# Kernel tuning notes

Measured on AMD Instinct MI355X. Metric: run time of the kernel, lower is better.

Reference implementation:

```python
import jax, jax.numpy as jnp
import numpy as np

B, T, D = 4, 2048, 2048
H = 16
HO = D // H  # head_out = 128


def setup_inputs() -> dict:
    key = jax.random.key(0)
    ks = jax.random.split(key, 6)
    x = jax.random.normal(ks[0], (B, T, D), dtype=jnp.float32)
    scale = 0.02
    Wq = jax.random.normal(ks[1], (D, D), dtype=jnp.float32) * scale
    Wk = jax.random.normal(ks[2], (D, D), dtype=jnp.float32) * scale
    Wv = jax.random.normal(ks[3], (D, D), dtype=jnp.float32) * scale
    Wp = jax.random.normal(ks[4], (D, D), dtype=jnp.float32) * scale
    bp = jnp.zeros((D,), dtype=jnp.float32)
    return {"x": x, "Wq": Wq, "Wk": Wk, "Wv": Wv, "Wp": Wp, "bp": bp}


def reference(x, Wq, Wk, Wv, Wp, bp):
    b, t, _ = x.shape
    # QKV projections (weights stored [d_in, d_out])
    q = x @ Wq
    k = x @ Wk
    v = x @ Wv
    split = lambda a: a.reshape(b, t, H, HO).transpose(0, 2, 1, 3)  # [b,H,T,ho]
    qh, kh, vh = split(q), split(k), split(v)
    # Feature attention: contract over tokens -> [b,H,ho,ho]
    scores = jnp.einsum('bhtf,bhtg->bhfg', qh, kh) / jnp.sqrt(jnp.float32(HO))
    weights = jax.nn.softmax(scores, axis=-1)  # dropout p=0.0 (identity)
    # feature_alibi: [1/T, 1/(T-1), ..., 1], broadcast over batch/head/feature
    feat_alibi = (1.0 / jnp.arange(t, 0, -1, dtype=jnp.float32)).reshape(1, 1, t, 1)
    vh = vh + feat_alibi
    # (weights @ v^T)^T : ctx[b,h,t,f] = sum_g weights[b,h,f,g] * v[b,h,t,g]
    ctx = jnp.einsum('bhfg,bhtg->bhtf', weights, vh)
    ctx = ctx.transpose(0, 2, 1, 3).reshape(b, t, H * HO)  # [b,T,d_out]
    return ctx @ Wp + bp
```

## Files before the change

### kernel.cpp

```cpp
#include <hip/hip_runtime.h>
#include <hip/hip_bf16.h>


#define Tt 2048
#define Dd 2048
#define Mm 8192

typedef __attribute__((ext_vector_type(4))) float f32x4;
typedef __attribute__((ext_vector_type(8))) short s16x8;
static_assert(sizeof(s16x8) == 16, "frag size");

typedef const __attribute__((address_space(1))) void* gptr_t;
typedef __attribute__((address_space(3))) void* lptr_t;

__device__ __forceinline__ float bf2f(ushort u) {
    union { unsigned int i; float f; } c; c.i = ((unsigned int)u) << 16; return c.f;
}
__device__ __forceinline__ ushort f2bf(float f) {
    union { float f; unsigned int i; } c; c.f = f;
    return (ushort)((c.i + 0x7FFFu + ((c.i >> 16) & 1u)) >> 16);
}
__device__ __forceinline__ void gload16(const void* g, void* l) {
    __builtin_amdgcn_global_load_lds((gptr_t)g, (lptr_t)l, 16, 0, 0);
}

#define MFMA_BF16(d, a, b) \
    asm("v_mfma_f32_16x16x32_bf16 %0, %1, %2, %0" : "+v"(d) : "v"(a), "v"(b))


__global__ __launch_bounds__(256) void convx_kernel(const float* __restrict__ x,
                                                    ushort* __restrict__ xb) {
    const int idx = blockIdx.x * 256 + threadIdx.x;
    const int stride = gridDim.x * 256;
    for (int i = idx; i < Mm * Dd / 4; i += stride) {
        const float4 v = *(const float4*)(x + (size_t)i * 4);
        ushort4 o; o.x = f2bf(v.x); o.y = f2bf(v.y); o.z = f2bf(v.z); o.w = f2bf(v.w);
        *(ushort4*)(xb + (size_t)i * 4) = o;
    }
}

__global__ __launch_bounds__(256) void transw_kernel(const float* __restrict__ W0,
        const float* __restrict__ W1, const float* __restrict__ W2,
        const float* __restrict__ W3, ushort* __restrict__ Wt) {
    __shared__ float tile[64][65];
    const int z = blockIdx.z;
    const float* W = (z == 0) ? W0 : (z == 1) ? W1 : (z == 2) ? W2 : W3;
    ushort* dst = Wt + (size_t)z * ((size_t)Dd * Dd);
    const int n0 = blockIdx.x * 64, k0 = blockIdx.y * 64;
    const int r4 = threadIdx.x >> 6, c = threadIdx.x & 63;
#pragma unroll
    for (int i = 0; i < 16; i++) {
        const int row = i * 4 + r4;
        tile[row][c] = W[(size_t)(k0 + row) * Dd + n0 + c];
    }
    __syncthreads();
#pragma unroll
    for (int i = 0; i < 16; i++) {
        const int row = i * 4 + r4;
        dst[(size_t)(n0 + row) * Dd + k0 + c] = f2bf(tile[c][row]);
    }
}


__device__ __forceinline__ void stage_half(char* ldsRegion, const ushort* gRegion,
                                           int ld, int half, int tid) {
#pragma unroll
    for (int j = 0; j < 2; j++) {
        const int Pb = half * 16384 + j * 8192 + (tid >> 6) * 1024;
        const int P = Pb + (tid & 63) * 16;
        const int row = P >> 7;
        const int colb = (P ^ ((row & 7) << 4)) & 127;
        gload16(gRegion + (size_t)row * ld + (colb >> 1), ldsRegion + Pb);
    }
}

template <int MODE>
__global__ __launch_bounds__(512, 2) void gemm256_kernel(
        const ushort* __restrict__ A, const ushort* __restrict__ Bt,
        void* __restrict__ Cv, const float* __restrict__ bias,
        int Kdim, int lda, int ldb, int ldc) {
    extern __shared__ char lds[];

    const int tid = threadIdx.x;
    const int w = tid >> 6, lane = tid & 63;
    const int wr = w >> 2, wc = w & 3;
    const int fr = lane & 15, fq = lane >> 4;

    const int bid = blockIdx.x;
    const int wg = (bid & 7) * 32 + (bid >> 3);
    const int m0 = (wg >> 3) * 256;
    const int n0 = (wg & 7) * 256;

    const ushort* Ag = A + (size_t)m0 * lda;
    const ushort* Bg = Bt + (size_t)n0 * ldb;
    const int NT = Kdim >> 6;

    const int aoff = wr * 16384 + fr * 128;
    const int boff = wc * 8192 + fr * 128;
    const int xo = (fr & 7) << 4;
    const int cp0 = (fq * 16) ^ xo;
    const int cp1 = (64 + fq * 16) ^ xo;

    f32x4 acc[8][4];
#pragma unroll
    for (int i = 0; i < 8; i++)
#pragma unroll
        for (int j = 0; j < 4; j++) acc[i][j] = {0.f, 0.f, 0.f, 0.f};

    {
        char* b0 = lds;
        char* b1 = lds + 65536;
        stage_half(b0,          Ag, lda, 0, tid);
        stage_half(b0,          Ag, lda, 1, tid);
        stage_half(b0 + 32768,  Bg, ldb, 0, tid);
        stage_half(b0 + 32768,  Bg, ldb, 1, tid);
        stage_half(b1 + 32768,  Bg + 64, ldb, 0, tid);
        stage_half(b1,          Ag + 64, lda, 0, tid);
        asm volatile("s_waitcnt vmcnt(4)" ::: "memory");
        __builtin_amdgcn_s_barrier();
    }

    s16x8 af[8];
    s16x8 bf[4][2];

    for (int t = 0; t < NT; ++t) {
        char* bufc = lds + (t & 1) * 65536;
        char* bufn = lds + ((t & 1) ^ 1) * 65536;

        if (t + 1 < NT) stage_half(bufn, Ag + (size_t)(t + 1) * 64, lda, 1, tid);
        {
            const char* pA = bufc + aoff + cp0;
#pragma unroll
            for (int mi = 0; mi < 8; mi++) af[mi] = *(const s16x8*)(pA + mi * 2048);
            const char* pB = bufc + 32768 + boff + cp0;
#pragma unroll
            for (int ni = 0; ni < 4; ni++) bf[ni][0] = *(const s16x8*)(pB + ni * 2048);
        }
        __builtin_amdgcn_sched_barrier(0);
        __builtin_amdgcn_s_barrier();
        asm volatile("s_waitcnt lgkmcnt(0)" ::: "memory");
        __builtin_amdgcn_sched_barrier(0);
        __builtin_amdgcn_s_setprio(1);
#pragma unroll
        for (int mi = 0; mi < 4; mi++)
#pragma unroll
            for (int ni = 0; ni < 4; ni++) MFMA_BF16(acc[mi][ni], af[mi], bf[ni][0]);
        __builtin_amdgcn_s_setprio(0);
        __builtin_amdgcn_sched_barrier(0);
        __builtin_amdgcn_s_barrier();

        if (t + 1 < NT) stage_half(bufn + 32768, Bg + (size_t)(t + 1) * 64, ldb, 1, tid);
        {
            const char* pB = bufc + 32768 + boff + cp1;
#pragma unroll
            for (int ni = 0; ni < 4; ni++) bf[ni][1] = *(const s16x8*)(pB + ni * 2048);
        }
        __builtin_amdgcn_sched_barrier(0);
        __builtin_amdgcn_s_barrier();
        asm volatile("s_waitcnt lgkmcnt(0)" ::: "memory");
        __builtin_amdgcn_sched_barrier(0);
        __builtin_amdgcn_s_setprio(1);
#pragma unroll
        for (int mi = 4; mi < 8; mi++)
#pragma unroll
            for (int ni = 0; ni < 4; ni++) MFMA_BF16(acc[mi][ni], af[mi], bf[ni][0]);
        __builtin_amdgcn_s_setprio(0);
        __builtin_amdgcn_sched_barrier(0);
        __builtin_amdgcn_s_barrier();

        if (t + 2 < NT) stage_half(bufc + 32768, Bg + (size_t)(t + 2) * 64, ldb, 0, tid);
        {
            const char* pA = bufc + aoff + cp1;
#pragma unroll
            for (int mi = 0; mi < 8; mi++) af[mi] = *(const s16x8*)(pA + mi * 2048);
        }
        __builtin_amdgcn_sched_barrier(0);
        __builtin_amdgcn_s_barrier();
        asm volatile("s_waitcnt lgkmcnt(0)" ::: "memory");
        __builtin_amdgcn_sched_barrier(0);
        __builtin_amdgcn_s_setprio(1);
#pragma unroll
        for (int mi = 0; mi < 4; mi++)
#pragma unroll
            for (int ni = 0; ni < 4; ni++) MFMA_BF16(acc[mi][ni], af[mi], bf[ni][1]);
        __builtin_amdgcn_s_setprio(0);
        __builtin_amdgcn_sched_barrier(0);
        __builtin_amdgcn_s_barrier();

        if (t + 2 < NT) stage_half(bufc, Ag + (size_t)(t + 2) * 64, lda, 0, tid);
        __builtin_amdgcn_sched_barrier(0);
        __builtin_amdgcn_s_setprio(1);
#pragma unroll
        for (int mi = 4; mi < 8; mi++)
#pragma unroll
            for (int ni = 0; ni < 4; ni++) MFMA_BF16(acc[mi][ni], af[mi], bf[ni][1]);
        __builtin_amdgcn_s_setprio(0);
        __builtin_amdgcn_sched_barrier(0);
        if (t < NT - 2) {
            asm volatile("s_waitcnt vmcnt(4)" ::: "memory");
        } else {
            asm volatile("s_waitcnt vmcnt(0)" ::: "memory");
        }
        __builtin_amdgcn_s_barrier();
    }

    asm volatile("s_nop 7\ns_nop 7\ns_nop 7");

    if (MODE == 2) {
        float* C = (float*)Cv;
#pragma unroll
        for (int mi = 0; mi < 8; mi++)
#pragma unroll
            for (int ni = 0; ni < 4; ni++)
#pragma unroll
                for (int r = 0; r < 4; r++) {
                    const int row = m0 + wr * 128 + mi * 16 + fq * 4 + r;
                    const int col = n0 + wc * 64 + ni * 16 + fr;
                    C[(size_t)row * ldc + col] = acc[mi][ni][r] + bias[col];
                }
    } else {
        ushort* C = (ushort*)Cv;
#pragma unroll
        for (int mi = 0; mi < 8; mi++)
#pragma unroll
            for (int ni = 0; ni < 4; ni++)
#pragma unroll
                for (int r = 0; r < 4; r++) {
                    const int row = m0 + wr * 128 + mi * 16 + fq * 4 + r;
                    const int col = n0 + wc * 64 + ni * 16 + fr;
                    C[(size_t)row * ldc + col] = f2bf(acc[mi][ni][r]);
                }
    }
}


template <int MODE>
__global__ __launch_bounds__(256, 2) void gemm_kernel(
        const ushort* __restrict__ A, const ushort* __restrict__ Bt,
        void* __restrict__ Cv, const float* __restrict__ bias,
        int Kdim, int lda, int ldb, int ldc) {
    __shared__ ushort lsA[128 * 32];
    __shared__ ushort lsB[128 * 32];

    const int tid = threadIdx.x;
    const int w = tid >> 6, lane = tid & 63;
    const int m0 = blockIdx.y * 128;
    const int n0 = blockIdx.x * 128;

    const ushort* Ab = A;
    const ushort* Bb = Bt;
    size_t coff = 0;
    if (MODE == 1) {
        const int z = blockIdx.z, b = z >> 4, h = z & 15;
        const size_t ao = (size_t)b * ((size_t)Tt * Dd) + (size_t)h * 128;
        Ab += ao; Bb += (size_t)z * (128 * 128); coff = ao;
    }

    const int sr = lane >> 2;
    const int sc = (lane & 3) * 8;
    const int c0 = w, c1 = w + 4;
    const int rA0 = c0 * 16 + sr, rA1 = c1 * 16 + sr;

    const int fr = lane & 15, fq = lane >> 4;
    const int wr = (w >> 1) * 64, wc = (w & 1) * 64;

    f32x4 acc[4][4];
#pragma unroll
    for (int i = 0; i < 4; i++)
#pragma unroll
        for (int j = 0; j < 4; j++) acc[i][j] = {0.f, 0.f, 0.f, 0.f};

    for (int kt = 0; kt < Kdim; kt += 32) {
        gload16(Ab + (size_t)(m0 + rA0) * lda + kt + sc, lsA + c0 * 512);
        gload16(Ab + (size_t)(m0 + rA1) * lda + kt + sc, lsA + c1 * 512);
        gload16(Bb + (size_t)(n0 + rA0) * ldb + kt + sc, lsB + c0 * 512);
        gload16(Bb + (size_t)(n0 + rA1) * ldb + kt + sc, lsB + c1 * 512);
        __syncthreads();

        s16x8 afrag[4], bfrag[4];
#pragma unroll
        for (int i = 0; i < 4; i++)
            afrag[i] = *(const s16x8*)(lsA + (wr + i * 16 + fr) * 32 + fq * 8);
#pragma unroll
        for (int j = 0; j < 4; j++)
            bfrag[j] = *(const s16x8*)(lsB + (wc + j * 16 + fr) * 32 + fq * 8);
#pragma unroll
        for (int i = 0; i < 4; i++)
#pragma unroll
            for (int j = 0; j < 4; j++)
                MFMA_BF16(acc[i][j], afrag[i], bfrag[j]);
        __syncthreads();
    }

    asm volatile("s_nop 7\ns_nop 7\ns_nop 7");

    {
        ushort* C = (ushort*)Cv + coff;
#pragma unroll
        for (int i = 0; i < 4; i++)
#pragma unroll
            for (int j = 0; j < 4; j++)
#pragma unroll
                for (int r = 0; r < 4; r++) {
                    const int row = m0 + wr + i * 16 + fq * 4 + r;
                    const int col = n0 + wc + j * 16 + fr;
                    float val = acc[i][j][r];
                    if (MODE == 1) val += 1.0f / (float)(Tt - row);
                    C[(size_t)row * ldc + col] = f2bf(val);
                }
    }
}


__global__ __launch_bounds__(256) void scores_kernel(const ushort* __restrict__ q,
        const ushort* __restrict__ k, float* __restrict__ part) {
    __shared__ float lsQ[32][128];
    __shared__ float lsK[32][128];
    const int tid = threadIdx.x;
    const int s = blockIdx.x, bh = blockIdx.y;
    const int b = bh >> 4, h = bh & 15;
    const size_t base = (size_t)b * ((size_t)Tt * Dd) + (size_t)h * 128;
    const ushort* qb = q + base;
    const ushort* kb = k + base;
    const int ty = tid >> 4, tx = tid & 15;
    const int f0 = ty * 8, g0 = tx * 8;

    float acc[8][8];
#pragma unroll
    for (int i = 0; i < 8; i++)
#pragma unroll
        for (int j = 0; j < 8; j++) acc[i][j] = 0.f;

    for (int ch = 0; ch < 8; ch++) {
        const int t0 = s * 256 + ch * 32;
#pragma unroll
        for (int ii = 0; ii < 4; ii++) {
            const int e = ii * 1024 + tid * 4;
            const int r = e >> 7, cc = e & 127;
            const size_t ga = (size_t)(t0 + r) * Dd + cc;
            const ushort4 v4 = *(const ushort4*)(qb + ga);
            f32x4 qf = {bf2f(v4.x), bf2f(v4.y), bf2f(v4.z), bf2f(v4.w)};
            *(f32x4*)&lsQ[r][cc] = qf;
            const ushort4 w4 = *(const ushort4*)(kb + ga);
            f32x4 kf = {bf2f(w4.x), bf2f(w4.y), bf2f(w4.z), bf2f(w4.w)};
            *(f32x4*)&lsK[r][cc] = kf;
        }
        __syncthreads();
#pragma unroll 4
        for (int tl = 0; tl < 32; tl++) {
            float qv[8], kv[8];
            *(f32x4*)&qv[0] = *(const f32x4*)&lsQ[tl][f0];
            *(f32x4*)&qv[4] = *(const f32x4*)&lsQ[tl][f0 + 4];
            *(f32x4*)&kv[0] = *(const f32x4*)&lsK[tl][g0];
            *(f32x4*)&kv[4] = *(const f32x4*)&lsK[tl][g0 + 4];
#pragma unroll
            for (int i = 0; i < 8; i++)
#pragma unroll
                for (int j = 0; j < 8; j++)
                    acc[i][j] = fmaf(qv[i], kv[j], acc[i][j]);
        }
        __syncthreads();
    }
    float* pb = part + ((size_t)s * 64 + bh) * 16384;
#pragma unroll
    for (int i = 0; i < 8; i++) {
        f32x4 o0 = {acc[i][0], acc[i][1], acc[i][2], acc[i][3]};
        f32x4 o1 = {acc[i][4], acc[i][5], acc[i][6], acc[i][7]};
        *(f32x4*)&pb[(f0 + i) * 128 + g0] = o0;
        *(f32x4*)&pb[(f0 + i) * 128 + g0 + 4] = o1;
    }
}


__global__ __launch_bounds__(256) void softmax_kernel(const float* __restrict__ part,
                                                      ushort* __restrict__ wts) {
    const int tid = threadIdx.x;
    const int wv = tid >> 6, lane = tid & 63;
    const int row = blockIdx.x * 4 + wv;
    const float* p = part + (size_t)row * 128 + lane * 2;
    float v0 = 0.f, v1 = 0.f;
#pragma unroll
    for (int s = 0; s < 8; s++) {
        const float2 t = *(const float2*)(p + (size_t)s * 1048576);
        v0 += t.x; v1 += t.y;
    }
    const float sc = 0.088388347648318447f;
    v0 *= sc; v1 *= sc;
    float m = fmaxf(v0, v1);
#pragma unroll
    for (int off = 32; off > 0; off >>= 1) m = fmaxf(m, __shfl_xor(m, off));
    const float e0 = __expf(v0 - m), e1 = __expf(v1 - m);
    float smv = e0 + e1;
#pragma unroll
    for (int off = 32; off > 0; off >>= 1) smv += __shfl_xor(smv, off);
    const float inv = 1.0f / smv;
    ushort2 o; o.x = f2bf(e0 * inv); o.y = f2bf(e1 * inv);
    *(ushort2*)(wts + (size_t)row * 128 + lane * 2) = o;
}


extern "C" void kernel_launch(void* const* d_in, const int* in_sizes, int n_in,
                              void* d_out, int out_size, void* d_ws, size_t ws_size,
                              hipStream_t stream) {
    const float* x  = (const float*)d_in[0];
    const float* Wq = (const float*)d_in[1];
    const float* Wk = (const float*)d_in[2];
    const float* Wv = (const float*)d_in[3];
    const float* Wp = (const float*)d_in[4];
    const float* bp = (const float*)d_in[5];
    float* out = (float*)d_out;
    char* ws = (char*)d_ws;

    ushort* xb   = (ushort*)(ws);
    ushort* Wt   = (ushort*)(ws + (33ull << 20));
    ushort* q    = (ushort*)(ws + (65ull << 20));
    ushort* k    = (ushort*)(ws + (97ull << 20));
    ushort* v    = (ushort*)(ws + (129ull << 20));
    float*  part = (float*) (ws + (161ull << 20));
    ushort* wts  = (ushort*)(ws + (193ull << 20));
    ushort* ctx  = xb;

    const size_t WSZ = (size_t)Dd * Dd;

    static_cast<void>(hipFuncSetAttribute((const void*)gemm256_kernel<0>,
        hipFuncAttributeMaxDynamicSharedMemorySize, 131072));
    static_cast<void>(hipFuncSetAttribute((const void*)gemm256_kernel<2>,
        hipFuncAttributeMaxDynamicSharedMemorySize, 131072));

    convx_kernel<<<2048, 256, 0, stream>>>(x, xb);
    transw_kernel<<<dim3(32, 32, 4), 256, 0, stream>>>(Wq, Wk, Wv, Wp, Wt);

    gemm256_kernel<0><<<256, 512, 131072, stream>>>(xb, Wt,           q, nullptr, 2048, 2048, 2048, 2048);
    gemm256_kernel<0><<<256, 512, 131072, stream>>>(xb, Wt + WSZ,     k, nullptr, 2048, 2048, 2048, 2048);
    gemm256_kernel<0><<<256, 512, 131072, stream>>>(xb, Wt + 2 * WSZ, v, nullptr, 2048, 2048, 2048, 2048);

    scores_kernel<<<dim3(8, 64), 256, 0, stream>>>(q, k, part);
    softmax_kernel<<<2048, 256, 0, stream>>>(part, wts);

    gemm_kernel<1><<<dim3(1, 16, 64), 256, 0, stream>>>(v, wts, ctx, nullptr, 128, 2048, 128, 2048);

    gemm256_kernel<2><<<256, 512, 131072, stream>>>(ctx, Wt + 3 * WSZ, out, bp, 2048, 2048, 2048, 2048);
}
```

Before: 382.6 us.

## Batch QKV GEMMs into one launch and restructure GEMM pipeline into quadrant phases

Measured after the change: 370.6 us. 1.03x faster.

```diff
diff --git a/kernel.cpp b/kernel.cpp
--- a/kernel.cpp
+++ b/kernel.cpp
@@ -23,6 +23,7 @@
 __device__ __forceinline__ void gload16(const void* g, void* l) {
     __builtin_amdgcn_global_load_lds((gptr_t)g, (lptr_t)l, 16, 0, 0);
 }
+__device__ __forceinline__ s16x8 ldfrag(const char* p) { return *(const s16x8*)p; }
 
 #define MFMA_BF16(d, a, b) \
     asm("v_mfma_f32_16x16x32_bf16 %0, %1, %2, %0" : "+v"(d) : "v"(a), "v"(b))
@@ -78,11 +79,13 @@
 __global__ __launch_bounds__(512, 2) void gemm256_kernel(
         const ushort* __restrict__ A, const ushort* __restrict__ Bt,
         void* __restrict__ Cv, const float* __restrict__ bias,
-        int Kdim, int lda, int ldb, int ldc) {
+        int Kdim, int lda, int ldb, int ldc,
+        size_t bstride, size_t cstride) {
     extern __shared__ char lds[];
 
     const int tid = threadIdx.x;
-    const int w = tid >> 6, lane = tid & 63;
+    const int lane = tid & 63;
+    const int w = tid >> 6;
     const int wr = w >> 2, wc = w & 3;
     const int fr = lane & 15, fq = lane >> 4;
 
@@ -92,7 +95,7 @@
     const int n0 = (wg & 7) * 256;
 
     const ushort* Ag = A + (size_t)m0 * lda;
-    const ushort* Bg = Bt + (size_t)n0 * ldb;
+    const ushort* Bg = Bt + (size_t)blockIdx.z * bstride + (size_t)n0 * ldb;
     const int NT = Kdim >> 6;
 
     const int aoff = wr * 16384 + fr * 128;
@@ -107,100 +110,124 @@
 #pragma unroll
         for (int j = 0; j < 4; j++) acc[i][j] = {0.f, 0.f, 0.f, 0.f};
 
+    s16x8 afX[4][2], afY[4][2], bf01[2][2], bf23[2][2];
+
     {
         char* b0 = lds;
         char* b1 = lds + 65536;
-        stage_half(b0,          Ag, lda, 0, tid);
-        stage_half(b0,          Ag, lda, 1, tid);
-        stage_half(b0 + 32768,  Bg, ldb, 0, tid);
-        stage_half(b0 + 32768,  Bg, ldb, 1, tid);
-        stage_half(b1 + 32768,  Bg + 64, ldb, 0, tid);
-        stage_half(b1,          Ag + 64, lda, 0, tid);
-        asm volatile("s_waitcnt vmcnt(4)" ::: "memory");
-        __builtin_amdgcn_s_barrier();
-    }
-
-    s16x8 af[8];
-    s16x8 bf[4][2];
+        stage_half(b0,         Ag, lda, 0, tid);
+        stage_half(b0,         Ag, lda, 1, tid);
+        stage_half(b0 + 32768, Bg, ldb, 0, tid);
+        stage_half(b0 + 32768, Bg, ldb, 1, tid);
+        if (NT > 1) {
+            stage_half(b1, Ag + 64, lda, 0, tid);
+            stage_half(b1, Ag + 64, lda, 1, tid);
+        }
+        __builtin_amdgcn_sched_barrier(0);
+        if (NT > 1) asm volatile("s_waitcnt vmcnt(4)" ::: "memory");
+        else        asm volatile("s_waitcnt vmcnt(0)" ::: "memory");
+        __builtin_amdgcn_s_barrier();
+        const char* Ab = b0 + aoff;
+        const char* Bb = b0 + 32768 + boff;
+#pragma unroll
+        for (int m = 0; m < 4; m++) {
+            afX[m][0] = ldfrag(Ab + m * 2048 + cp0);
+            afX[m][1] = ldfrag(Ab + m * 2048 + cp1);
+        }
+#pragma unroll
+        for (int n = 0; n < 2; n++) {
+            bf01[n][0] = ldfrag(Bb + n * 2048 + cp0);
+            bf01[n][1] = ldfrag(Bb + n * 2048 + cp1);
+        }
+        __builtin_amdgcn_sched_barrier(0);
+    }
 
     for (int t = 0; t < NT; ++t) {
         char* bufc = lds + (t & 1) * 65536;
         char* bufn = lds + ((t & 1) ^ 1) * 65536;
-
-        if (t + 1 < NT) stage_half(bufn, Ag + (size_t)(t + 1) * 64, lda, 1, tid);
-        {
-            const char* pA = bufc + aoff + cp0;
-#pragma unroll
-            for (int mi = 0; mi < 8; mi++) af[mi] = *(const s16x8*)(pA + mi * 2048);
-            const char* pB = bufc + 32768 + boff + cp0;
-#pragma unroll
-            for (int ni = 0; ni < 4; ni++) bf[ni][0] = *(const s16x8*)(pB + ni * 2048);
-        }
-        __builtin_amdgcn_sched_barrier(0);
-        __builtin_amdgcn_s_barrier();
+        const char* Ab = bufc + aoff;
+        const char* Bb = bufc + 32768 + boff;
+
+#pragma unroll
+        for (int n = 0; n < 2; n++) {
+            bf23[n][0] = ldfrag(Bb + (n + 2) * 2048 + cp0);
+            bf23[n][1] = ldfrag(Bb + (n + 2) * 2048 + cp1);
+        }
+        if (t + 1 < NT) stage_half(bufn + 32768, Bg + (size_t)(t + 1) * 64, ldb, 0, tid);
+        __builtin_amdgcn_sched_barrier(0);
+        __builtin_amdgcn_s_barrier();
+        asm volatile("s_waitcnt lgkmcnt(4)" ::: "memory");
+        __builtin_amdgcn_s_setprio(1);
+#pragma unroll
+        for (int k = 0; k < 2; k++)
+#pragma unroll
+            for (int m = 0; m < 4; m++)
+#pragma unroll
+                for (int n = 0; n < 2; n++) MFMA_BF16(acc[m][n], afX[m][k], bf01[n][k]);
+        __builtin_amdgcn_s_setprio(0);
+        __builtin_amdgcn_s_barrier();
+
+#pragma unroll
+        for (int m = 0; m < 4; m++) {
+            afY[m][0] = ldfrag(Ab + (m + 4) * 2048 + cp0);
+            afY[m][1] = ldfrag(Ab + (m + 4) * 2048 + cp1);
+        }
+        if (t + 1 < NT) stage_half(bufn + 32768, Bg + (size_t)(t + 1) * 64, ldb, 1, tid);
+        __builtin_amdgcn_sched_barrier(0);
+        __builtin_amdgcn_s_barrier();
+        asm volatile("s_waitcnt lgkmcnt(8)" ::: "memory");
+        __builtin_amdgcn_s_setprio(1);
+#pragma unroll
+        for (int k = 0; k < 2; k++)
+#pragma unroll
+            for (int m = 0; m < 4; m++)
+#pragma unroll
+                for (int n = 0; n < 2; n++) MFMA_BF16(acc[m][n + 2], afX[m][k], bf23[n][k]);
+        __builtin_amdgcn_s_setprio(0);
+        __builtin_amdgcn_s_barrier();
+
         asm volatile("s_waitcnt lgkmcnt(0)" ::: "memory");
-        __builtin_amdgcn_sched_barrier(0);
         __builtin_amdgcn_s_setprio(1);
 #pragma unroll
-        for (int mi = 0; mi < 4; mi++)
-#pragma unroll
-            for (int ni = 0; ni < 4; ni++) MFMA_BF16(acc[mi][ni], af[mi], bf[ni][0]);
+        for (int k = 0; k < 2; k++)
+#pragma unroll
+            for (int m = 0; m < 4; m++)
+#pragma unroll
+                for (int n = 0; n < 2; n++) MFMA_BF16(acc[m + 4][n], afY[m][k], bf01[n][k]);
         __builtin_amdgcn_s_setprio(0);
-        __builtin_amdgcn_sched_barrier(0);
-        __builtin_amdgcn_s_barrier();
-
-        if (t + 1 < NT) stage_half(bufn + 32768, Bg + (size_t)(t + 1) * 64, ldb, 1, tid);
-        {
-            const char* pB = bufc + 32768 + boff + cp1;
-#pragma unroll
-            for (int ni = 0; ni < 4; ni++) bf[ni][1] = *(const s16x8*)(pB + ni * 2048);
-        }
-        __builtin_amdgcn_sched_barrier(0);
-        __builtin_amdgcn_s_barrier();
-        asm volatile("s_waitcnt lgkmcnt(0)" ::: "memory");
+        __builtin_amdgcn_s_barrier();
+
+        if (t + 2 < NT) {
+            stage_half(bufc, Ag + (size_t)(t + 2) * 64, lda, 0, tid);
+            stage_half(bufc, Ag + (size_t)(t + 2) * 64, lda, 1, tid);
+        }
+        __builtin_amdgcn_sched_barrier(0);
+        if (t + 2 < NT) asm volatile("s_waitcnt vmcnt(4)" ::: "memory");
+        else            asm volatile("s_waitcnt vmcnt(0)" ::: "memory");
+        __builtin_amdgcn_s_barrier();
+        if (t + 1 < NT) {
+            const char* nAb = bufn + aoff;
+            const char* nBb = bufn + 32768 + boff;
+#pragma unroll
+            for (int m = 0; m < 4; m++) {
+                afX[m][0] = ldfrag(nAb + m * 2048 + cp0);
+                afX[m][1] = ldfrag(nAb + m * 2048 + cp1);
+            }
+#pragma unroll
+            for (int n = 0; n < 2; n++) {
+                bf01[n][0] = ldfrag(nBb + n * 2048 + cp0);
+                bf01[n][1] = ldfrag(nBb + n * 2048 + cp1);
+            }
+        }
         __builtin_amdgcn_sched_barrier(0);
         __builtin_amdgcn_s_setprio(1);
 #pragma unroll
-        for (int mi = 4; mi < 8; mi++)
-#pragma unroll
-            for (int ni = 0; ni < 4; ni++) MFMA_BF16(acc[mi][ni], af[mi], bf[ni][0]);
+        for (int k = 0; k < 2; k++)
+#pragma unroll
+            for (int m = 0; m < 4; m++)
+#pragma unroll
+                for (int n = 0; n < 2; n++) MFMA_BF16(acc[m + 4][n + 2], afY[m][k], bf23[n][k]);
         __builtin_amdgcn_s_setprio(0);
-        __builtin_amdgcn_sched_barrier(0);
-        __builtin_amdgcn_s_barrier();
-
-        if (t + 2 < NT) stage_half(bufc + 32768, Bg + (size_t)(t + 2) * 64, ldb, 0, tid);
-        {
-            const char* pA = bufc + aoff + cp1;
-#pragma unroll
-            for (int mi = 0; mi < 8; mi++) af[mi] = *(const s16x8*)(pA + mi * 2048);
-        }
-        __builtin_amdgcn_sched_barrier(0);
-        __builtin_amdgcn_s_barrier();
-        asm volatile("s_waitcnt lgkmcnt(0)" ::: "memory");
-        __builtin_amdgcn_sched_barrier(0);
-        __builtin_amdgcn_s_setprio(1);
-#pragma unroll
-        for (int mi = 0; mi < 4; mi++)
-#pragma unroll
-            for (int ni = 0; ni < 4; ni++) MFMA_BF16(acc[mi][ni], af[mi], bf[ni][1]);
-        __builtin_amdgcn_s_setprio(0);
-        __builtin_amdgcn_sched_barrier(0);
-        __builtin_amdgcn_s_barrier();
-
-        if (t + 2 < NT) stage_half(bufc, Ag + (size_t)(t + 2) * 64, lda, 0, tid);
-        __builtin_amdgcn_sched_barrier(0);
-        __builtin_amdgcn_s_setprio(1);
-#pragma unroll
-        for (int mi = 4; mi < 8; mi++)
-#pragma unroll
-            for (int ni = 0; ni < 4; ni++) MFMA_BF16(acc[mi][ni], af[mi], bf[ni][1]);
-        __builtin_amdgcn_s_setprio(0);
-        __builtin_amdgcn_sched_barrier(0);
-        if (t < NT - 2) {
-            asm volatile("s_waitcnt vmcnt(4)" ::: "memory");
-        } else {
-            asm volatile("s_waitcnt vmcnt(0)" ::: "memory");
-        }
         __builtin_amdgcn_s_barrier();
     }
 
@@ -219,7 +246,7 @@
                     C[(size_t)row * ldc + col] = acc[mi][ni][r] + bias[col];
                 }
     } else {
-        ushort* C = (ushort*)Cv;
+        ushort* C = (ushort*)Cv + (size_t)blockIdx.z * cstride;
 #pragma unroll
         for (int mi = 0; mi < 8; mi++)
 #pragma unroll
@@ -421,6 +448,7 @@
     ushort* ctx  = xb;
 
     const size_t WSZ = (size_t)Dd * Dd;
+    const size_t QSTRIDE = (32ull << 20) / 2;
 
     static_cast<void>(hipFuncSetAttribute((const void*)gemm256_kernel<0>,
         hipFuncAttributeMaxDynamicSharedMemorySize, 131072));
@@ -430,14 +458,14 @@
     convx_kernel<<<2048, 256, 0, stream>>>(x, xb);
     transw_kernel<<<dim3(32, 32, 4), 256, 0, stream>>>(Wq, Wk, Wv, Wp, Wt);
 
-    gemm256_kernel<0><<<256, 512, 131072, stream>>>(xb, Wt,           q, nullptr, 2048, 2048, 2048, 2048);
-    gemm256_kernel<0><<<256, 512, 131072, stream>>>(xb, Wt + WSZ,     k, nullptr, 2048, 2048, 2048, 2048);
-    gemm256_kernel<0><<<256, 512, 131072, stream>>>(xb, Wt + 2 * WSZ, v, nullptr, 2048, 2048, 2048, 2048);
+    gemm256_kernel<0><<<dim3(256, 1, 3), 512, 131072, stream>>>(
+        xb, Wt, q, nullptr, 2048, 2048, 2048, 2048, WSZ, QSTRIDE);
 
     scores_kernel<<<dim3(8, 64), 256, 0, stream>>>(q, k, part);
     softmax_kernel<<<2048, 256, 0, stream>>>(part, wts);
 
     gemm_kernel<1><<<dim3(1, 16, 64), 256, 0, stream>>>(v, wts, ctx, nullptr, 128, 2048, 128, 2048);
 
-    gemm256_kernel<2><<<256, 512, 131072, stream>>>(ctx, Wt + 3 * WSZ, out, bp, 2048, 2048, 2048, 2048);
-}
+    gemm256_kernel<2><<<dim3(256, 1, 1), 512, 131072, stream>>>(
+        ctx, Wt + 3 * WSZ, out, bp, 2048, 2048, 2048, 2048, 0, 0);
+}
```
